# Performance work log

Hardware: AMD Instinct MI355X
Metric: run time of the kernel (lower is better)

Reference implementation:

```python
import jax, jax.numpy as jnp
import numpy as np

WALK_LENGTH = 8
NUM_WALKS = 5
BIRTH_DEATH_EPS = 0.1
TOLERANCE = 0.1
HALF_WIN = 16          # window is [cur-16, cur+17)
TEMP = 5.0
NEG = -1e9
EPS = 1e-8


def setup_inputs() -> dict:
    key = jax.random.key(0)
    k1, k2 = jax.random.split(key)
    seq_len, hidden = 8192, 1024
    hidden_states = jax.random.normal(k1, (seq_len, hidden), dtype=jnp.float32)
    violation_indices = jax.random.randint(k2, (1024,), 0, seq_len)
    return {"hidden_states": hidden_states, "violation_indices": violation_indices}


def _cycle_ok(row_sq, i, j, k):
    # TriadicReciprocityCheck.check_cycle, simplified algebraically:
    # M_ab = outer(b,a)/|a|^2 etc., so P = M_ca M_bc M_ab
    #      = outer(a,a) * |b|^2 |c|^2 / ((|a|^2+eps)(|b|^2+eps)(|c|^2+eps))
    # => trace(P) == fro_norm(P) == |a|^2|b|^2|c|^2 / denom  (outer(a,a) has trace=fro=|a|^2)
    na, nb, nc = row_sq[i], row_sq[j], row_sq[k]
    tr = na * nb * nc / ((na + EPS) * (nb + EPS) * (nc + EPS))
    dev = jnp.abs(tr - jnp.round(tr))
    return (dev <= TOLERANCE) & (tr <= 1.5)


def _walk(key, start, states_norm, row_sq, violation_indices):
    seq_len = states_norm.shape[0]
    offsets = jnp.arange(-HALF_WIN, HALF_WIN + 1)  # 33 local positions

    def step(carry, _):
        key, cur, prev, plen, min_sim, done, detected, aborts, restarts = carry
        key, k_samp, k_restart = jax.random.split(key, 3)
        idxs = cur + offsets
        valid = (idxs >= 0) & (idxs < seq_len)
        g = states_norm[jnp.clip(idxs, 0, seq_len - 1)]      # [33, D]
        sims = g @ states_norm[cur]                           # [33]
        logits = jnp.where(valid & (idxs != cur), sims, NEG) * TEMP
        # up to 3 multinomial attempts, each gated by the triadic reciprocity check
        samp_keys = jax.random.split(k_samp, 3)
        picks = jax.vmap(lambda k: jax.random.categorical(k, logits))(samp_keys)
        cands = cur + offsets[picks]                          # [3] candidate nodes
        ok = jax.vmap(lambda c: (plen < 2) | _cycle_ok(row_sq, prev, cur, c))(cands)
        found = jnp.any(ok)
        first = jnp.argmax(ok)
        n_aborts = jnp.where(found, first, 3).astype(jnp.int32)  # failed attempts
        cand = cands[first]
        # 'jump mental tracks': teleport to a random violation node if all attempts fail
        r = jax.random.randint(k_restart, (), 0, violation_indices.shape[0])
        restart_node = violation_indices[r]
        sim = states_norm[cur] @ states_norm[cand]
        new_min = jnp.minimum(min_sim, sim)  # path_sims min (NOT reset on restart)
        closed = found & (cand == start) & (plen > 2)
        act = ~done
        aborts = aborts + jnp.where(act, n_aborts, 0).astype(jnp.int32)
        restarts = restarts + jnp.where(act & ~found, 1, 0).astype(jnp.int32)
        detected = detected | (act & closed & (new_min < BIRTH_DEATH_EPS))
        done = done | (act & closed)
        cur2 = jnp.where(found, cand, restart_node)
        prev2 = jnp.where(found, cur, restart_node)
        plen2 = jnp.where(found, plen + 1, 1).astype(jnp.int32)
        ms2 = jnp.where(found, new_min, min_sim)
        cur = jnp.where(act, cur2, cur)
        prev = jnp.where(act, prev2, prev)
        plen = jnp.where(act, plen2, plen)
        min_sim = jnp.where(act, ms2, min_sim)
        return (key, cur, prev, plen, min_sim, done, detected, aborts, restarts), None

    init = (key, start, start, jnp.int32(1), jnp.float32(1e9),
            jnp.bool_(False), jnp.bool_(False), jnp.int32(0), jnp.int32(0))
    carry, _ = jax.lax.scan(step, init, None, length=WALK_LENGTH)
    return carry[6], carry[7], carry[8]  # detected, aborts, restarts


def reference(hidden_states, violation_indices):
    states_norm = hidden_states / (jnp.linalg.norm(hidden_states, axis=1, keepdims=True) + EPS)
    row_sq = jnp.sum(hidden_states * hidden_states, axis=1)  # |h_i|^2, for cycle check
    nv = violation_indices.shape[0]
    keys = jax.random.split(jax.random.key(42), nv * NUM_WALKS).reshape(nv, NUM_WALKS)
    walk = lambda k, s: _walk(k, s, states_norm, row_sq, violation_indices)
    det, ab, rs = jax.vmap(lambda ks, s: jax.vmap(lambda k: walk(k, s))(ks))(keys, violation_indices)
    instability_detected = jnp.any(det, axis=1)  # [num_violations] bool
    return instability_detected, jnp.sum(ab), jnp.sum(rs)
```

## Files before the change

### kernel.cpp

```cpp
#include <hip/hip_runtime.h>
#include <stdint.h>
#include <math.h>


#define HID        1024
#define NUM_WALKS  5
#define WALK_LEN   8
#define HALF_WIN   16
#define E_THRESH_F 1.6487213f

#define CENTERS    16
#define SROWS      32
#define KHALF      512

__device__ __forceinline__ void tf2x32(uint32_t k0, uint32_t k1,
                                       uint32_t& x0, uint32_t& x1) {
  uint32_t ks2 = k0 ^ k1 ^ 0x1BD11BDAu;
  x0 += k0; x1 += k1;
#define TFR(r) { x0 += x1; x1 = (x1 << (r)) | (x1 >> (32 - (r))); x1 ^= x0; }
  TFR(13) TFR(15) TFR(26) TFR(6)
  x0 += k1;  x1 += ks2 + 1u;
  TFR(17) TFR(29) TFR(16) TFR(24)
  x0 += ks2; x1 += k0 + 2u;
  TFR(13) TFR(15) TFR(26) TFR(6)
  x0 += k0;  x1 += k1 + 3u;
  TFR(17) TFR(29) TFR(16) TFR(24)
  x0 += k1;  x1 += ks2 + 4u;
  TFR(13) TFR(15) TFR(26) TFR(6)
  x0 += ks2; x1 += k0 + 5u;
#undef TFR
}

__device__ __forceinline__ uint32_t tf_fold(uint32_t k0, uint32_t k1,
                                            uint32_t c0, uint32_t c1) {
  tf2x32(k0, k1, c0, c1);
  return c0 ^ c1;
}

__device__ __forceinline__ double fast_neg_log(uint32_t bits) {
  const uint32_t k = bits >> 9;
  if (k == 0) return 87.33654475055310899;
  const float u  = (float)k * 1.1920928955078125e-7f;
  const float l2 = __log2f(u);
  return (double)l2 * -0.6931471805599453;
}

__global__ __launch_bounds__(512) void band_fused_kernel(
    const float* __restrict__ H, float* __restrict__ sumsqf,
    float* __restrict__ Ef, int* __restrict__ out, int out_n, int seq_len) {
  __shared__ __align__(16) float  tile[SROWS][KHALF];
  __shared__ double ssq[SROWS];

  if (blockIdx.x == 0) {
    for (int t = threadIdx.x; t < out_n; t += 512) out[t] = 0;
  }

  int wg = blockIdx.x;
  {
    const int nwg = gridDim.x;
    if ((nwg & 7) == 0) wg = (wg & 7) * (nwg >> 3) + (wg >> 3);
  }
  const int wid  = (int)(threadIdx.x >> 6);
  const int lane = (int)(threadIdx.x & 63);
  const int i0   = wg * CENTERS;
  const float4* __restrict__ H4 = (const float4*)H;

  double acc[4]  = {0.0, 0.0, 0.0, 0.0};
  double dsum[2] = {0.0, 0.0};

#pragma unroll
  for (int half = 0; half < 2; ++half) {
#pragma unroll
    for (int rr = 0; rr < 4; ++rr) {
      const int local = wid * 4 + rr;
      const int row   = i0 + local;
      if (row < seq_len) {
        const float4* src = H4 + ((size_t)row << 8);
        float4* dst = (float4*)&tile[local][0];
#pragma unroll
        for (int kk = 0; kk < 2; ++kk) {
          float4 x = src[lane + ((half * 2 + kk) << 6)];
          dst[lane + (kk << 6)] = x;
          acc[rr] += (double)x.x * x.x + (double)x.y * x.y
                   + (double)x.z * x.z + (double)x.w * x.w;
        }
      }
    }
    if (half == 1) {
#pragma unroll
      for (int rr = 0; rr < 4; ++rr) {
        const int local = wid * 4 + rr;
        const int row   = i0 + local;
        if (row < seq_len) {
          double a = acc[rr];
#pragma unroll
          for (int off = 32; off; off >>= 1) a += __shfl_xor(a, off);
          if (lane == 0) {
            ssq[local] = a;
            if (local < CENTERS)
              sumsqf[row] = (float)a;
          }
        }
      }
    }
    __syncthreads();

#pragma unroll
    for (int cc = 0; cc < 2; ++cc) {
      const int cl = wid * 2 + cc;
      const int i  = i0 + cl;
      if (i >= seq_len) continue;

      float a[8];
      {
        const float4* rc = (const float4*)&tile[cl][0];
#pragma unroll
        for (int kk = 0; kk < 2; ++kk) {
          float4 x = rc[lane + (kk << 6)];
          a[4*kk+0] = x.x; a[4*kk+1] = x.y; a[4*kk+2] = x.z; a[4*kk+3] = x.w;
        }
      }

      double p[16];
#pragma unroll
      for (int d = 1; d <= 16; ++d) {
        const float4* rb = (const float4*)&tile[cl + d][0];
        float ps = 0.0f;
#pragma unroll
        for (int kk = 0; kk < 2; ++kk) {
          float4 x = rb[lane + (kk << 6)];
          ps += a[4*kk+0] * x.x + a[4*kk+1] * x.y
              + a[4*kk+2] * x.z + a[4*kk+3] * x.w;
        }
        p[d-1] = (double)ps;
      }

#pragma unroll
      for (int v = 0; v < 8; ++v) {
        double send = (lane & 32) ? p[v] : p[v+8];
        double recv = __shfl_xor(send, 32);
        double mine = (lane & 32) ? p[v+8] : p[v];
        p[v] = mine + recv;
      }
#pragma unroll
      for (int v = 0; v < 4; ++v) {
        double send = (lane & 16) ? p[v] : p[v+4];
        double recv = __shfl_xor(send, 16);
        double mine = (lane & 16) ? p[v+4] : p[v];
        p[v] = mine + recv;
      }
#pragma unroll
      for (int v = 0; v < 2; ++v) {
        double send = (lane & 8) ? p[v] : p[v+2];
        double recv = __shfl_xor(send, 8);
        double mine = (lane & 8) ? p[v+2] : p[v];
        p[v] = mine + recv;
      }
      {
        double send = (lane & 4) ? p[0] : p[1];
        double recv = __shfl_xor(send, 4);
        double mine = (lane & 4) ? p[1] : p[0];
        p[0] = mine + recv;
      }
      p[0] += __shfl_xor(p[0], 2);
      p[0] += __shfl_xor(p[0], 1);

      dsum[cc] += p[0];
    }
    __syncthreads();
  }

  const int v = ((lane >> 2) & 1) | (((lane >> 3) & 1) << 1)
              | (((lane >> 4) & 1) << 2) | (((lane >> 5) & 1) << 3);
  const int d = v + 1;
#pragma unroll
  for (int cc = 0; cc < 2; ++cc) {
    const int cl = wid * 2 + cc;
    const int i  = i0 + cl;
    if (i < seq_len && (lane & 3) == 0 && i + d < seq_len) {
      const double ni = sqrt(ssq[cl]) + 1e-8;
      const double s  = dsum[cc] / (ni * (sqrt(ssq[cl + d]) + 1e-8));
      const float  Ev = (float)exp(5.0 * s);
      Ef[(size_t)i * 33 + 16 + d]       = Ev;
      Ef[(size_t)(i + d) * 33 + 16 - d] = Ev;
    }
  }
}

__global__ __launch_bounds__(256) void rowsq_kernel(
    const float* __restrict__ H, double* __restrict__ sumsq,
    int* __restrict__ out, int out_n, int seq_len) {
  if (blockIdx.x == 0) {
    for (int t = threadIdx.x; t < out_n; t += 256) out[t] = 0;
  }
  const int row  = (int)((blockIdx.x * blockDim.x + threadIdx.x) >> 6);
  const int lane = threadIdx.x & 63;
  if (row >= seq_len) return;
  const float4* r = (const float4*)(H + (size_t)row * HID);
  double acc = 0.0;
#pragma unroll
  for (int k = 0; k < 4; ++k) {
    float4 x = r[lane + (k << 6)];
    acc += (double)x.x * x.x + (double)x.y * x.y
         + (double)x.z * x.z + (double)x.w * x.w;
  }
#pragma unroll
  for (int off = 32; off; off >>= 1) acc += __shfl_xor(acc, off);
  if (lane == 0) sumsq[row] = acc;
}

__global__ __launch_bounds__(256) void walk_pre_kernel(
    const float* __restrict__ Ef, const float* __restrict__ sumsqf,
    const int* __restrict__ viol, int* __restrict__ out,
    int nv, int seq_len) {
  int wave = (int)((blockIdx.x * blockDim.x + threadIdx.x) >> 6);
  const int lane = threadIdx.x & 63;
  if (wave >= nv * NUM_WALKS) return;
  wave = __builtin_amdgcn_readfirstlane(wave);
  const int v     = wave / NUM_WALKS;
  const int start = viol[v];

  uint32_t key0 = 0u, key1 = (uint32_t)wave;
  tf2x32(0u, 42u, key0, key1);
  key0 = __builtin_amdgcn_readfirstlane(key0);
  key1 = __builtin_amdgcn_readfirstlane(key1);

  uint32_t k0s[WALK_LEN], k1s[WALK_LEN];
#pragma unroll
  for (int s = 0; s < WALK_LEN; ++s) {
    k0s[s] = key0; k1s[s] = key1;
    uint32_t nk0 = 0u, nk1 = 0u; tf2x32(key0, key1, nk0, nk1);
    key0 = __builtin_amdgcn_readfirstlane(nk0);
    key1 = __builtin_amdgcn_readfirstlane(nk1);
  }

  const int  sl_mine = lane & 31;
  const uint32_t jpk = (uint32_t)(sl_mine + (sl_mine > 15 ? 1 : 0));
  float invwp[WALK_LEN / 2];
#pragma unroll
  for (int t = 0; t < WALK_LEN / 2; ++t) {
    uint32_t ksA0 = 0u, ksA1 = 1u; tf2x32(k0s[2*t],   k1s[2*t],   ksA0, ksA1);
    uint32_t sA0  = 0u, sA1  = 0u; tf2x32(ksA0, ksA1, sA0, sA1);
    uint32_t ksB0 = 0u, ksB1 = 1u; tf2x32(k0s[2*t+1], k1s[2*t+1], ksB0, ksB1);
    uint32_t sB0  = 0u, sB1  = 0u; tf2x32(ksB0, ksB1, sB0, sB1);
    const uint32_t s0 = (lane & 32) ? sB0 : sA0;
    const uint32_t s1 = (lane & 32) ? sB1 : sA1;
    const uint32_t bits = tf_fold(s0, s1, 0u, jpk);
    invwp[t] = (float)(1.0 / fast_neg_log(bits));
  }

  const int sl_use = (lane < 33 && lane != HALF_WIN)
                   ? (lane - (lane > HALF_WIN)) : 0;

  int   cur = start, prev = start, plen = 1;
  float minE = 1e30f;
  bool  detected = false;
  int   aborts = 0, restarts = 0;
  float na_f = sumsqf[start], nb_f = na_f;

#pragma unroll
  for (int step = 0; step < WALK_LEN; ++step) {
    const int  myidx   = cur - HALF_WIN + lane;
    const bool myvalid = (lane < 33) && (lane != HALF_WIN) &&
                         (myidx >= 0) && (myidx < seq_len);
    const int  clipped = myidx < 0 ? 0 : (myidx >= seq_len ? seq_len - 1 : myidx);
    const float Ejf    = Ef[(size_t)cur * 33 + (lane < 33 ? lane : 0)];
    const float sq_win = sumsqf[clipped];
    const float invw_s = __shfl(invwp[step >> 1],
                                ((step & 1) << 5) + sl_use);

    bool found = false; int fails = 0, p = 0, cand = 0;
    float nc_f = 0.0f;
    for (int at = 0; at < 3; ++at) {
      float f; int bi;
      if (myvalid) {
        if (at == 0) {
          f = Ejf * invw_s;
        } else {
          uint32_t ks0 = 0u, ks1 = 1u; tf2x32(k0s[step], k1s[step], ks0, ks1);
          uint32_t s0 = 0u, s1 = (uint32_t)at; tf2x32(ks0, ks1, s0, s1);
          const uint32_t bits = tf_fold(s0, s1, 0u, (uint32_t)lane);
          f = (float)((double)Ejf / fast_neg_log(bits));
        }
        bi = lane;
      } else { f = -1.0f; bi = 1000; }
#pragma unroll
      for (int off = 32; off; off >>= 1) {
        const float of = __shfl_xor(f, off);
        const int   oi = __shfl_xor(bi, off);
        if (of > f || (of == f && oi < bi)) { f = of; bi = oi; }
      }
      p    = bi;
      cand = cur - HALF_WIN + p;
      nc_f = __shfl(sq_win, p);
      bool ok;
      if (plen < 2) ok = true;
      else {
        const float na = na_f, nb = nb_f, nc = nc_f;
        const float tr  = (na * nb * nc) /
                          ((na + 1e-8f) * (nb + 1e-8f) * (nc + 1e-8f));
        const float dev = fabsf(tr - rintf(tr));
        ok = (dev <= 0.1f) && (tr <= 1.5f);
      }
      if (ok) { found = true; break; }
      ++fails;
    }
    aborts += fails;

    if (found) {
      const float Ewin = __shfl(Ejf, p);
      minE = fminf(minE, Ewin);
      const bool closed = (cand == start) && (plen > 2);
      prev = cur; cur = cand; plen += 1;
      na_f = nb_f; nb_f = nc_f;
      if (closed) { if (minE < E_THRESH_F) detected = true; break; }
    } else {
      ++restarts;
      uint32_t kr0 = 0u, kr1 = 2u; tf2x32(k0s[step], k1s[step], kr0, kr1);
      uint32_t h0 = 0u, h1 = 0u; tf2x32(kr0, kr1, h0, h1);
      uint32_t l0 = 0u, l1 = 1u; tf2x32(kr0, kr1, l0, l1);
      const uint32_t hi = tf_fold(h0, h1, 0u, 0u);
      const uint32_t lo = tf_fold(l0, l1, 0u, 0u);
      const uint32_t span = (uint32_t)nv;
      uint32_t mult = (65536u % span); mult = (mult * mult) % span;
      const uint32_t r = ((hi % span) * mult + (lo % span)) % span;
      const int node = viol[r];
      cur = node; prev = node; plen = 1;
      na_f = sumsqf[node]; nb_f = na_f;
    }
  }

  if (lane == 0) {
    if (detected)      atomicOr(&out[v], 1);
    if (aborts != 0)   atomicAdd(&out[nv], aborts);
    if (restarts != 0) atomicAdd(&out[nv + 1], restarts);
  }
}

__global__ __launch_bounds__(256) void walk_ref_kernel(
    const float* __restrict__ H, const int* __restrict__ viol,
    const double* __restrict__ sumsq, int* __restrict__ out,
    int nv, int seq_len) {
  const int wave = (int)((blockIdx.x * blockDim.x + threadIdx.x) >> 6);
  const int lane = threadIdx.x & 63;
  if (wave >= nv * NUM_WALKS) return;
  const int v     = wave / NUM_WALKS;
  const int start = viol[v];
  uint32_t key0 = 0u, key1 = (uint32_t)wave;
  tf2x32(0u, 42u, key0, key1);
  const float4* __restrict__ H4 = (const float4*)H;
  int    cur = start, prev = start, plen = 1;
  double min_sim = 1e9;
  bool   detected = false;
  int    aborts = 0, restarts = 0;
  for (int step = 0; step < WALK_LEN; ++step) {
    uint32_t nk0 = 0u, nk1 = 0u; tf2x32(key0, key1, nk0, nk1);
    uint32_t ks0 = 0u, ks1 = 1u; tf2x32(key0, key1, ks0, ks1);
    uint32_t kr0 = 0u, kr1 = 2u; tf2x32(key0, key1, kr0, kr1);
    const double ncur = sqrt(sumsq[cur]) + 1e-8;
    double a[16];
    {
      const float4* rc = H4 + ((size_t)cur << 8);
#pragma unroll
      for (int k = 0; k < 4; ++k) {
        float4 x = rc[lane + (k << 6)];
        a[4*k+0] = x.x; a[4*k+1] = x.y; a[4*k+2] = x.z; a[4*k+3] = x.w;
      }
    }
    double my_sim = 0.0;
    for (int jj = 0; jj < 33; ++jj) {
      const int idx = cur - HALF_WIN + jj;
      if (jj == HALF_WIN || idx < 0 || idx >= seq_len) continue;
      const float4* rb = H4 + ((size_t)idx << 8);
      double acc = 0.0;
#pragma unroll
      for (int k = 0; k < 4; ++k) {
        float4 x = rb[lane + (k << 6)];
        acc += a[4*k+0] * (double)x.x + a[4*k+1] * (double)x.y
             + a[4*k+2] * (double)x.z + a[4*k+3] * (double)x.w;
      }
#pragma unroll
      for (int off = 32; off; off >>= 1) acc += __shfl_xor(acc, off);
      const double s = acc / (ncur * (sqrt(sumsq[idx]) + 1e-8));
      if (lane == jj) my_sim = s;
    }
    bool found = false; int fails = 0, p = 0, cand = 0;
    const int  myidx   = cur - HALF_WIN + lane;
    const bool myvalid = (lane < 33) && (lane != HALF_WIN) &&
                         (myidx >= 0) && (myidx < seq_len);
    for (int at = 0; at < 3; ++at) {
      uint32_t s0 = 0u, s1 = (uint32_t)at; tf2x32(ks0, ks1, s0, s1);
      double z; int bi;
      if (myvalid) {
        const uint32_t bits = tf_fold(s0, s1, 0u, (uint32_t)lane);
        const uint32_t fb   = (bits >> 9) | 0x3f800000u;
        const float    f    = __uint_as_float(fb) - 1.0f;
        const float    u    = (f > 0.0f) ? f : 1.1754943508222875e-38f;
        const double   g    = -log(-log((double)u));
        z  = g + 5.0 * my_sim;
        bi = lane;
      } else { z = -1e300; bi = 1000; }
#pragma unroll
      for (int off = 32; off; off >>= 1) {
        const double oz = __shfl_xor(z, off);
        const int    oi = __shfl_xor(bi, off);
        if (oz > z || (oz == z && oi < bi)) { z = oz; bi = oi; }
      }
      p    = bi;
      cand = cur - HALF_WIN + p;
      bool ok;
      if (plen < 2) ok = true;
      else {
        const float na = (float)sumsq[prev], nb = (float)sumsq[cur],
                    nc = (float)sumsq[cand];
        const float tr  = (na * nb * nc) /
                          ((na + 1e-8f) * (nb + 1e-8f) * (nc + 1e-8f));
        const float dev = fabsf(tr - rintf(tr));
        ok = (dev <= 0.1f) && (tr <= 1.5f);
      }
      if (ok) { found = true; break; }
      ++fails;
    }
    aborts += fails;
    if (found) {
      const double sim = __shfl(my_sim, p);
      const double nm  = fmin(min_sim, sim);
      const bool closed = (cand == start) && (plen > 2);
      prev = cur; cur = cand; plen += 1; min_sim = nm;
      if (closed) { if (nm < 0.1) detected = true; break; }
    } else {
      ++restarts;
      uint32_t h0 = 0u, h1 = 0u; tf2x32(kr0, kr1, h0, h1);
      uint32_t l0 = 0u, l1 = 1u; tf2x32(kr0, kr1, l0, l1);
      const uint32_t hi = tf_fold(h0, h1, 0u, 0u);
      const uint32_t lo = tf_fold(l0, l1, 0u, 0u);
      const uint32_t span = (uint32_t)nv;
      uint32_t mult = (65536u % span); mult = (mult * mult) % span;
      const uint32_t r = ((hi % span) * mult + (lo % span)) % span;
      const int node = viol[r];
      cur = node; prev = node; plen = 1;
    }
    key0 = nk0; key1 = nk1;
  }
  if (lane == 0) {
    if (detected)      atomicOr(&out[v], 1);
    if (aborts != 0)   atomicAdd(&out[nv], aborts);
    if (restarts != 0) atomicAdd(&out[nv + 1], restarts);
  }
}

extern "C" void kernel_launch(void* const* d_in, const int* in_sizes, int n_in,
                              void* d_out, int out_size, void* d_ws, size_t ws_size,
                              hipStream_t stream) {
  const float* H    = (const float*)d_in[0];
  const int*   viol = (const int*)d_in[1];
  const int    nv      = in_sizes[1];
  const int    seq_len = in_sizes[0] / HID;
  const int    nwalks  = nv * NUM_WALKS;

  float* sumsqf = (float*)d_ws;
  float* Etabf  = (float*)((char*)d_ws + (size_t)seq_len * sizeof(float));
  const size_t need = (size_t)seq_len * sizeof(float)
                    + (size_t)seq_len * 33 * sizeof(float);

  const int wblocks = (nwalks + 3) / 4;

  if (ws_size >= need) {
    const int blocks = (seq_len + CENTERS - 1) / CENTERS;
    band_fused_kernel<<<blocks, 512, 0, stream>>>(H, sumsqf, Etabf,
                                                  (int*)d_out, out_size,
                                                  seq_len);
    walk_pre_kernel<<<wblocks, 256, 0, stream>>>(Etabf, sumsqf, viol,
                                                 (int*)d_out, nv, seq_len);
  } else {
    double* sumsq = (double*)d_ws;
    const int blocks = (seq_len + 3) / 4;
    rowsq_kernel<<<blocks, 256, 0, stream>>>(H, sumsq, (int*)d_out,
                                             out_size, seq_len);
    walk_ref_kernel<<<wblocks, 256, 0, stream>>>(H, viol, sumsq,
                                                 (int*)d_out, nv, seq_len);
  }
}
```

Before: 52.41 us.

## Precompute first-attempt sampling weights in band kernel tail for walk kernel

The band kernel gets a tail phase that computes the first-attempt Gumbel/exponential inverse weights for every walk step and stores them in a workspace table. A new walk kernel reads these weights instead of running the threefry chains on its serial critical path. Only retries and restarts still generate random numbers inline. This moves RNG work off the latency-bound walk kernel and into the wide band kernel, at the cost of extra workspace, extra global writes and reads, and a longer band kernel.

```diff
diff --git a/kernel.cpp b/kernel.cpp
--- a/kernel.cpp
+++ b/kernel.cpp
@@ -45,9 +45,38 @@
   return (double)l2 * -0.6931471805599453;
 }
 
+__device__ __forceinline__ void produce_w(float* __restrict__ Wtab,
+                                          int wk, int lane) {
+  uint32_t k0 = 0u, k1 = (uint32_t)wk;
+  tf2x32(0u, 42u, k0, k1);
+  k0 = __builtin_amdgcn_readfirstlane(k0);
+  k1 = __builtin_amdgcn_readfirstlane(k1);
+  const int sl = lane & 31;
+  const uint32_t jpk = (uint32_t)(sl + (sl > 15 ? 1 : 0));
+#pragma unroll
+  for (int t = 0; t < WALK_LEN / 2; ++t) {
+    uint32_t ksA0 = 0u, ksA1 = 1u; tf2x32(k0, k1, ksA0, ksA1);
+    uint32_t n0   = 0u, n1   = 0u; tf2x32(k0, k1, n0, n1);
+    n0 = __builtin_amdgcn_readfirstlane(n0);
+    n1 = __builtin_amdgcn_readfirstlane(n1);
+    uint32_t ksB0 = 0u, ksB1 = 1u; tf2x32(n0, n1, ksB0, ksB1);
+    uint32_t m0   = 0u, m1   = 0u; tf2x32(n0, n1, m0, m1);
+    uint32_t sA0  = 0u, sA1  = 0u; tf2x32(ksA0, ksA1, sA0, sA1);
+    uint32_t sB0  = 0u, sB1  = 0u; tf2x32(ksB0, ksB1, sB0, sB1);
+    const uint32_t s0 = (lane & 32) ? sB0 : sA0;
+    const uint32_t s1 = (lane & 32) ? sB1 : sA1;
+    const uint32_t bits = tf_fold(s0, s1, 0u, jpk);
+    const float invw = (float)(1.0 / fast_neg_log(bits));
+    Wtab[(((size_t)wk * WALK_LEN + 2 * t + (lane >> 5)) << 5) + sl] = invw;
+    k0 = __builtin_amdgcn_readfirstlane(m0);
+    k1 = __builtin_amdgcn_readfirstlane(m1);
+  }
+}
+
 __global__ __launch_bounds__(512) void band_fused_kernel(
     const float* __restrict__ H, float* __restrict__ sumsqf,
-    float* __restrict__ Ef, int* __restrict__ out, int out_n, int seq_len) {
+    float* __restrict__ Ef, float* __restrict__ Wtab, int nwalks,
+    int* __restrict__ out, int out_n, int seq_len) {
   __shared__ __align__(16) float  tile[SROWS][KHALF];
   __shared__ double ssq[SROWS];
 
@@ -185,6 +214,13 @@
       Ef[(size_t)(i + d) * 33 + 16 - d] = Ev;
     }
   }
+
+  if (Wtab != nullptr) {
+    const int gw     = (int)blockIdx.x * 8 + wid;
+    const int stride = (int)gridDim.x * 8;
+    for (int wk = gw; wk < nwalks; wk += stride)
+      produce_w(Wtab, wk, lane);
+  }
 }
 
 __global__ __launch_bounds__(256) void rowsq_kernel(
@@ -207,6 +243,120 @@
 #pragma unroll
   for (int off = 32; off; off >>= 1) acc += __shfl_xor(acc, off);
   if (lane == 0) sumsq[row] = acc;
+}
+
+__global__ __launch_bounds__(256) void walk_tab_kernel(
+    const float* __restrict__ Ef, const float* __restrict__ sumsqf,
+    const float* __restrict__ Wtab, const int* __restrict__ viol,
+    int* __restrict__ out, int nv, int seq_len) {
+  int wave = (int)((blockIdx.x * blockDim.x + threadIdx.x) >> 6);
+  const int lane = threadIdx.x & 63;
+  if (wave >= nv * NUM_WALKS) return;
+  wave = __builtin_amdgcn_readfirstlane(wave);
+  const int v     = wave / NUM_WALKS;
+  const int start = viol[v];
+
+  uint32_t key0 = 0u, key1 = (uint32_t)wave;
+  tf2x32(0u, 42u, key0, key1);
+  key0 = __builtin_amdgcn_readfirstlane(key0);
+  key1 = __builtin_amdgcn_readfirstlane(key1);
+
+  uint32_t k0s[WALK_LEN], k1s[WALK_LEN];
+#pragma unroll
+  for (int s = 0; s < WALK_LEN; ++s) {
+    k0s[s] = key0; k1s[s] = key1;
+    uint32_t nk0 = 0u, nk1 = 0u; tf2x32(key0, key1, nk0, nk1);
+    key0 = __builtin_amdgcn_readfirstlane(nk0);
+    key1 = __builtin_amdgcn_readfirstlane(nk1);
+  }
+
+  const int sl_use = (lane < 33 && lane != HALF_WIN)
+                   ? (lane - (lane > HALF_WIN)) : 0;
+  const float* __restrict__ Wrow =
+      Wtab + (((size_t)wave * WALK_LEN) << 5) + sl_use;
+
+  int   cur = start, prev = start, plen = 1;
+  float minE = 1e30f;
+  bool  detected = false;
+  int   aborts = 0, restarts = 0;
+  float na_f = sumsqf[start], nb_f = na_f;
+
+#pragma unroll
+  for (int step = 0; step < WALK_LEN; ++step) {
+    const int  myidx   = cur - HALF_WIN + lane;
+    const bool myvalid = (lane < 33) && (lane != HALF_WIN) &&
+                         (myidx >= 0) && (myidx < seq_len);
+    const int  clipped = myidx < 0 ? 0 : (myidx >= seq_len ? seq_len - 1 : myidx);
+    const float Ejf    = Ef[(size_t)cur * 33 + (lane < 33 ? lane : 0)];
+    const float sq_win = sumsqf[clipped];
+    const float invw_s = Wrow[(size_t)step << 5];
+
+    bool found = false; int fails = 0, p = 0, cand = 0;
+    float nc_f = 0.0f;
+    for (int at = 0; at < 3; ++at) {
+      float f; int bi;
+      if (myvalid) {
+        if (at == 0) {
+          f = Ejf * invw_s;
+        } else {
+          uint32_t ks0 = 0u, ks1 = 1u; tf2x32(k0s[step], k1s[step], ks0, ks1);
+          uint32_t s0 = 0u, s1 = (uint32_t)at; tf2x32(ks0, ks1, s0, s1);
+          const uint32_t bits = tf_fold(s0, s1, 0u, (uint32_t)lane);
+          f = (float)((double)Ejf / fast_neg_log(bits));
+        }
+        bi = lane;
+      } else { f = -1.0f; bi = 1000; }
+#pragma unroll
+      for (int off = 32; off; off >>= 1) {
+        const float of = __shfl_xor(f, off);
+        const int   oi = __shfl_xor(bi, off);
+        if (of > f || (of == f && oi < bi)) { f = of; bi = oi; }
+      }
+      p    = bi;
+      cand = cur - HALF_WIN + p;
+      nc_f = __shfl(sq_win, p);
+      bool ok;
+      if (plen < 2) ok = true;
+      else {
+        const float na = na_f, nb = nb_f, nc = nc_f;
+        const float tr  = (na * nb * nc) /
+                          ((na + 1e-8f) * (nb + 1e-8f) * (nc + 1e-8f));
+        const float dev = fabsf(tr - rintf(tr));
+        ok = (dev <= 0.1f) && (tr <= 1.5f);
+      }
+      if (ok) { found = true; break; }
+      ++fails;
+    }
+    aborts += fails;
+
+    if (found) {
+      const float Ewin = __shfl(Ejf, p);
+      minE = fminf(minE, Ewin);
+      const bool closed = (cand == start) && (plen > 2);
+      prev = cur; cur = cand; plen += 1;
+      na_f = nb_f; nb_f = nc_f;
+      if (closed) { if (minE < E_THRESH_F) detected = true; break; }
+    } else {
+      ++restarts;
+      uint32_t kr0 = 0u, kr1 = 2u; tf2x32(k0s[step], k1s[step], kr0, kr1);
+      uint32_t h0 = 0u, h1 = 0u; tf2x32(kr0, kr1, h0, h1);
+      uint32_t l0 = 0u, l1 = 1u; tf2x32(kr0, kr1, l0, l1);
+      const uint32_t hi = tf_fold(h0, h1, 0u, 0u);
+      const uint32_t lo = tf_fold(l0, l1, 0u, 0u);
+      const uint32_t span = (uint32_t)nv;
+      uint32_t mult = (65536u % span); mult = (mult * mult) % span;
+      const uint32_t r = ((hi % span) * mult + (lo % span)) % span;
+      const int node = viol[r];
+      cur = node; prev = node; plen = 1;
+      na_f = sumsqf[node]; nb_f = na_f;
+    }
+  }
+
+  if (lane == 0) {
+    if (detected)      atomicOr(&out[v], 1);
+    if (aborts != 0)   atomicAdd(&out[nv], aborts);
+    if (restarts != 0) atomicAdd(&out[nv + 1], restarts);
+  }
 }
 
 __global__ __launch_bounds__(256) void walk_pre_kernel(
@@ -460,16 +610,26 @@
 
   float* sumsqf = (float*)d_ws;
   float* Etabf  = (float*)((char*)d_ws + (size_t)seq_len * sizeof(float));
-  const size_t need = (size_t)seq_len * sizeof(float)
-                    + (size_t)seq_len * 33 * sizeof(float);
+  const size_t need2 = (size_t)seq_len * sizeof(float)
+                     + (size_t)seq_len * 33 * sizeof(float);
+  float* Wtabf  = (float*)((char*)d_ws + ((need2 + 255) & ~(size_t)255));
+  const size_t needW = ((need2 + 255) & ~(size_t)255)
+                     + (size_t)nwalks * WALK_LEN * 32 * sizeof(float);
 
   const int wblocks = (nwalks + 3) / 4;
 
-  if (ws_size >= need) {
+  if (ws_size >= needW) {
     const int blocks = (seq_len + CENTERS - 1) / CENTERS;
-    band_fused_kernel<<<blocks, 512, 0, stream>>>(H, sumsqf, Etabf,
-                                                  (int*)d_out, out_size,
-                                                  seq_len);
+    band_fused_kernel<<<blocks, 512, 0, stream>>>(H, sumsqf, Etabf, Wtabf,
+                                                  nwalks, (int*)d_out,
+                                                  out_size, seq_len);
+    walk_tab_kernel<<<wblocks, 256, 0, stream>>>(Etabf, sumsqf, Wtabf, viol,
+                                                 (int*)d_out, nv, seq_len);
+  } else if (ws_size >= need2) {
+    const int blocks = (seq_len + CENTERS - 1) / CENTERS;
+    band_fused_kernel<<<blocks, 512, 0, stream>>>(H, sumsqf, Etabf, nullptr,
+                                                  nwalks, (int*)d_out,
+                                                  out_size, seq_len);
     walk_pre_kernel<<<wblocks, 256, 0, stream>>>(Etabf, sumsqf, viol,
                                                  (int*)d_out, nv, seq_len);
   } else {
```

Result: slower. 60.61 us (+15.7%).
